# Kernel optimization log

Measured on AMD Instinct MI355X. Metric: run time of the kernel, lower is better.

## Reference

```python
import jax, jax.numpy as jnp
import numpy as np

B, S, D, H = 4, 2048, 1024, 16
NEG = -1e10  # matches the module's -10000000000.0 additive mask


def setup_inputs() -> dict:
    key = jax.random.key(0)
    k1, k2, k3, k4, k5 = jax.random.split(key, 5)
    scale = 0.02
    return {
        "x": jax.random.normal(k1, (B, S, D), dtype=jnp.float32),
        "w_qkv": jax.random.normal(k2, (D, 3 * D), dtype=jnp.float32) * scale,
        "b_qkv": jax.random.normal(k3, (3 * D,), dtype=jnp.float32) * scale,
        "w_out": jax.random.normal(k4, (D, D), dtype=jnp.float32) * scale,
        "b_out": jax.random.normal(k5, (D,), dtype=jnp.float32) * scale,
    }


def reference(x, w_qkv, b_qkv, w_out, b_out):
    b, s, d = x.shape
    hd = d // H  # per-head dim
    qkv = x @ w_qkv + b_qkv  # [b,s,3d]
    qq, kk, vv = jnp.split(qkv, 3, axis=-1)
    # [b,h,s,hd]
    qq = qq.reshape(b, s, H, hd).transpose(0, 2, 1, 3)
    kk = kk.reshape(b, s, H, hd).transpose(0, 2, 1, 3)
    vv = vv.reshape(b, s, H, hd).transpose(0, 2, 1, 3)
    scale = 1.0 / float(hd) ** 0.5
    # additive causal mask: NEG above diagonal, 0 on/below (as in module)
    mask = (1.0 - jnp.tri(s, dtype=jnp.float32)) * NEG
    attn = jnp.einsum("bhqd,bhkd->bhqk", qq, kk) * scale + mask
    attn = jax.nn.softmax(attn, axis=-1)
    out = jnp.einsum("bhqk,bhkd->bhqd", attn, vv)  # [b,h,s,hd]
    out = out.transpose(0, 2, 1, 3).reshape(b, s, d)
    return out @ w_out + b_out
```

## Files before the change

### kernel.cpp

```cpp
#include <hip/hip_runtime.h>
#include <hip/hip_bf16.h>
#include <stdint.h>


#define B_   4
#define S_   2048
#define D_   1024
#define H_   16
#define HD_  64
#define MTOK (B_ * S_)
#define BK   32
#define QSCALE 0.18033688011112042f

typedef __attribute__((ext_vector_type(8))) short bfx8;
typedef __attribute__((ext_vector_type(4))) float fx4;
typedef __attribute__((ext_vector_type(16))) float fx16;

static __device__ __forceinline__ unsigned short f2bf(float f) {
    union { float f; uint32_t u; } v{f};
    uint32_t u = v.u;
    u += 0x7fffu + ((u >> 16) & 1u);
    return (unsigned short)(u >> 16);
}

static __device__ __forceinline__ uint32_t cvtpk(float lo, float hi) {
    uint32_t r;
    asm volatile("v_cvt_pk_bf16_f32 %0, %1, %2" : "=v"(r) : "v"(lo), "v"(hi));
    return r;
}

static __device__ __forceinline__ void pswap(uint32_t& a, uint32_t& b) {
    asm volatile("v_permlane32_swap_b32 %0, %1" : "+v"(a), "+v"(b));
}

static __device__ __forceinline__ void gll16(const unsigned short* g, const unsigned short* l) {
    typedef const __attribute__((address_space(1))) void* gp_t;
    typedef __attribute__((address_space(3))) void* lp_t;
    __builtin_amdgcn_global_load_lds((gp_t)(uintptr_t)g, (lp_t)(uint32_t)(uintptr_t)l, 16, 0, 0);
}

__global__ void k_conv_x(const float* __restrict__ x, unsigned short* __restrict__ xb, int n8) {
    int i = blockIdx.x * blockDim.x + threadIdx.x;
    int stride = gridDim.x * blockDim.x;
    for (; i < n8; i += stride) {
        const float4* p = (const float4*)(x + (size_t)i * 8);
        float4 a = p[0], b = p[1];
        bfx8 o;
        o[0]=f2bf(a.x); o[1]=f2bf(a.y); o[2]=f2bf(a.z); o[3]=f2bf(a.w);
        o[4]=f2bf(b.x); o[5]=f2bf(b.y); o[6]=f2bf(b.z); o[7]=f2bf(b.w);
        *(bfx8*)(xb + (size_t)i * 8) = o;
    }
}

__global__ void k_transpose_bf(const float* __restrict__ w, unsigned short* __restrict__ wt,
                               int K, int N) {
    int idx = blockIdx.x * blockDim.x + threadIdx.x;
    int total = N * (K / 8);
    if (idx >= total) return;
    int n  = idx % N;
    int k0 = (idx / N) * 8;
    bfx8 o;
#pragma unroll
    for (int j = 0; j < 8; ++j) o[j] = f2bf(w[(size_t)(k0 + j) * N + n]);
    *(bfx8*)(wt + (size_t)n * K + k0) = o;
}

__global__ void k_transpose_v(const unsigned short* __restrict__ Vw,
                              unsigned short* __restrict__ Vt) {
    __shared__ unsigned short lds[64][72];
    const int bg = blockIdx.x;
    const int bh = bg >> 5;
    const int st = (bg & 31) * 64;
    const int t = threadIdx.x;
#pragma unroll
    for (int j = 0; j < 2; ++j) {
        int c = t + 256 * j;
        int row = c >> 3, q = c & 7;
        *(bfx8*)&lds[row][q * 8] = *(const bfx8*)&Vw[((size_t)bh * S_ + st + row) * HD_ + q * 8];
    }
    __syncthreads();
#pragma unroll
    for (int j = 0; j < 2; ++j) {
        int c = t + 256 * j;
        int d = c >> 3, q = c & 7;
        bfx8 o;
#pragma unroll
        for (int e = 0; e < 8; ++e) o[e] = lds[q * 8 + e][d];
        *(bfx8*)&Vt[((size_t)bh * HD_ + d) * S_ + st + q * 8] = o;
    }
}

__launch_bounds__(256)
__global__ void k_gemm_qkv(const unsigned short* __restrict__ A,
                           const unsigned short* __restrict__ Bt,
                           const float* __restrict__ bias,
                           unsigned short* __restrict__ Qw,
                           unsigned short* __restrict__ Kw,
                           unsigned short* __restrict__ Vw) {
    __shared__ unsigned short Al[128 * BK];
    __shared__ unsigned short Bl[128 * BK];
    const int wg = blockIdx.x;
    const int lin = (wg & 7) * 192 + (wg >> 3);
    const int ny = lin / 24, nx = lin - ny * 24;
    const int m0 = ny * 128;
    const int n0 = nx * 128;
    const int t = threadIdx.x;
    const int w = t >> 6, l = t & 63;
    const int wr = w >> 1, wc = w & 1;
    const int lr = l & 15, lg = l >> 4;
    const int srow = l >> 2;
    const int scol = (l & 3) * 8;
    fx4 acc[4][4] = {};

    for (int k0 = 0; k0 < D_; k0 += BK) {
        __syncthreads();
#pragma unroll
        for (int j = 0; j < 2; ++j) {
            int rb = j * 64 + w * 16;
            gll16(&A [(size_t)(m0 + rb + srow) * D_ + k0 + scol], &Al[rb * BK]);
            gll16(&Bt[(size_t)(n0 + rb + srow) * D_ + k0 + scol], &Bl[rb * BK]);
        }
        __syncthreads();
        bfx8 af[4], bf[4];
#pragma unroll
        for (int i = 0; i < 4; ++i) af[i] = *(const bfx8*)&Al[(wr * 64 + i * 16 + lr) * BK + lg * 8];
#pragma unroll
        for (int i = 0; i < 4; ++i) bf[i] = *(const bfx8*)&Bl[(wc * 64 + i * 16 + lr) * BK + lg * 8];
#pragma unroll
        for (int mi = 0; mi < 4; ++mi)
#pragma unroll
            for (int ni = 0; ni < 4; ++ni)
                acc[mi][ni] = __builtin_amdgcn_mfma_f32_16x16x32_bf16(bf[ni], af[mi], acc[mi][ni], 0, 0, 0);
    }

#pragma unroll
    for (int ni = 0; ni < 4; ++ni) {
        const int nn = n0 + wc * 64 + ni * 16 + lg * 4;
        const int mat = nn >> 10;
        const int h = (nn & 1023) >> 6, dd = nn & 63;
        const float4 bv = *(const float4*)&bias[nn];
        unsigned short* dst = (mat == 0) ? Qw : (mat == 1) ? Kw : Vw;
        const float sc = (mat == 0) ? QSCALE : 1.0f;
#pragma unroll
        for (int mi = 0; mi < 4; ++mi) {
            const int m = m0 + wr * 64 + mi * 16 + lr;
            const int b = m >> 11, s = m & 2047;
            const int bh = b * H_ + h;
            fx4 v = acc[mi][ni];
            float o0 = (v[0] + bv.x) * sc, o1 = (v[1] + bv.y) * sc;
            float o2 = (v[2] + bv.z) * sc, o3 = (v[3] + bv.w) * sc;
            uint2 u; u.x = cvtpk(o0, o1); u.y = cvtpk(o2, o3);
            *(uint2*)&dst[((size_t)bh * S_ + s) * HD_ + dd] = u;
        }
    }
}

__launch_bounds__(512, 4)
__global__ void k_attn(const unsigned short* __restrict__ Qw,
                       const unsigned short* __restrict__ Kw,
                       const unsigned short* __restrict__ Vt,
                       unsigned short* __restrict__ Ob) {
    __shared__ unsigned short Kl[2][64 * 64];
    __shared__ unsigned short Vl[2][64 * 64];
    const int wg = blockIdx.x;
    const int xcd = wg & 7, ix = wg >> 3;
    const int bh = xcd * 8 + (ix >> 3);
    const int pi = ix & 7;
    const int t = threadIdx.x;
    const int w = t >> 6, l = t & 63;
    const int lq = l & 31, hi = l >> 5;
    const int tile = (w < 4) ? (15 - pi) : pi;
    const int qr = tile * 128 + (w & 3) * 32;
    const int NT = 32 - 2 * pi;

    const unsigned short* Qp = Qw + (size_t)bh * S_ * HD_;
    const unsigned short* Kp = Kw + (size_t)bh * S_ * HD_;
    const unsigned short* Vp = Vt + (size_t)bh * HD_ * S_;

    bfx8 qf[4];
#pragma unroll
    for (int kb = 0; kb < 4; ++kb)
        qf[kb] = *(const bfx8*)&Qp[(size_t)(qr + lq) * HD_ + kb * 16 + hi * 8];

    fx16 oacc[2] = {};
    float mrow = -1e30f, lsum = 0.f;

    auto pvstep = [&](const uint32_t* pk, int s, int cb, int buf) {
        uint32_t w0 = pk[4 * s], w1 = pk[4 * s + 1], w2 = pk[4 * s + 2], w3 = pk[4 * s + 3];
        pswap(w0, w2);
        pswap(w1, w3);
        union { uint32_t u[4]; bfx8 v; } pf;
        pf.u[0] = w0; pf.u[1] = w1; pf.u[2] = w2; pf.u[3] = w3;
        bfx8 v0 = *(const bfx8*)((const char*)&Vl[buf][0] + lq * 128 + (cb ^ ((lq & 7) << 4)));
        bfx8 v1 = *(const bfx8*)((const char*)&Vl[buf][0] + (32 + lq) * 128 + (cb ^ ((lq & 7) << 4)));
        oacc[0] = __builtin_amdgcn_mfma_f32_32x32x16_bf16(v0, pf.v, oacc[0], 0, 0, 0);
        oacc[1] = __builtin_amdgcn_mfma_f32_32x32x16_bf16(v1, pf.v, oacc[1], 0, 0, 0);
    };

    {
        bfx8 sreg[2];
#pragma unroll
        for (int it = 0; it < 2; ++it) {
            int id = t + 512 * it;
            int c = id & 511;
            int row = c >> 3, q = c & 7;
            if (id < 512) sreg[it] = *(const bfx8*)&Kp[(size_t)row * HD_ + q * 8];
            else          sreg[it] = *(const bfx8*)&Vp[(size_t)row * S_ + q * 8];
        }
#pragma unroll
        for (int it = 0; it < 2; ++it) {
            int id = t + 512 * it;
            int c = id & 511;
            int row = c >> 3, q = c & 7;
            int off = row * 128 + ((q * 16) ^ ((row & 7) << 4));
            char* base = (id < 512) ? (char*)&Kl[0][0] : (char*)&Vl[0][0];
            *(bfx8*)(base + off) = sreg[it];
        }
    }
    __syncthreads();

    int buf = 0;
    for (int tkv = 0; tkv < NT; ++tkv) {
        const int kv0 = tkv * 64;
        const bool pre = (tkv + 1 < NT);
        bfx8 sreg[2];
        if (pre) {
            const int kn = kv0 + 64;
#pragma unroll
            for (int it = 0; it < 2; ++it) {
                int id = t + 512 * it;
                int c = id & 511;
                int row = c >> 3, q = c & 7;
                if (id < 512) sreg[it] = *(const bfx8*)&Kp[(size_t)(kn + row) * HD_ + q * 8];
                else          sreg[it] = *(const bfx8*)&Vp[(size_t)row * S_ + kn + q * 8];
            }
        }
        if (kv0 <= qr + 31) {
            fx16 s0 = {}, s1 = {};
            __builtin_amdgcn_s_setprio(1);
#pragma unroll
            for (int kb = 0; kb < 4; ++kb) {
                const int cb = kb * 32 + hi * 16;
                bfx8 k0 = *(const bfx8*)((const char*)&Kl[buf][0] + lq * 128 + (cb ^ ((lq & 7) << 4)));
                bfx8 k1 = *(const bfx8*)((const char*)&Kl[buf][0] + (32 + lq) * 128 + (cb ^ ((lq & 7) << 4)));
                s0 = __builtin_amdgcn_mfma_f32_32x32x16_bf16(k0, qf[kb], s0, 0, 0, 0);
                s1 = __builtin_amdgcn_mfma_f32_32x32x16_bf16(k1, qf[kb], s1, 0, 0, 0);
            }
            __builtin_amdgcn_s_setprio(0);
            if (kv0 + 63 > qr) {
                const int qrel = qr + lq - kv0;
#pragma unroll
                for (int r = 0; r < 16; ++r) {
                    const int kvo = (r & 3) + 8 * (r >> 2) + 4 * hi;
                    if (kvo > qrel)      s0[r] = -1e30f;
                    if (kvo + 32 > qrel) s1[r] = -1e30f;
                }
            }
            float mx = fmaxf(s0[0], s1[0]);
#pragma unroll
            for (int r = 1; r < 16; ++r) mx = fmaxf(mx, fmaxf(s0[r], s1[r]));
            mx = fmaxf(mx, __shfl_xor(mx, 32));
            if (!__all(mx <= mrow + 8.f)) {
                const float mnew = fmaxf(mrow, mx);
                const float al = exp2f(mrow - mnew);
                mrow = mnew;
#pragma unroll
                for (int r = 0; r < 16; ++r) { oacc[0][r] *= al; oacc[1][r] *= al; }
                lsum *= al;
            }
            uint32_t pk0[8], pk1[8];
            float ps = 0.f;
#pragma unroll
            for (int j = 0; j < 8; ++j) {
                float a0 = exp2f(s0[2 * j] - mrow), b0 = exp2f(s0[2 * j + 1] - mrow);
                float a1 = exp2f(s1[2 * j] - mrow), b1 = exp2f(s1[2 * j + 1] - mrow);
                ps += (a0 + b0) + (a1 + b1);
                pk0[j] = cvtpk(a0, b0);
                pk1[j] = cvtpk(a1, b1);
            }
            lsum += ps + __shfl_xor(ps, 32);
            __builtin_amdgcn_s_setprio(1);
            pvstep(pk0, 0, 0 * 32 + hi * 16, buf);
            pvstep(pk0, 1, 1 * 32 + hi * 16, buf);
            pvstep(pk1, 0, 2 * 32 + hi * 16, buf);
            pvstep(pk1, 1, 3 * 32 + hi * 16, buf);
            __builtin_amdgcn_s_setprio(0);
        }
        if (pre) {
#pragma unroll
            for (int it = 0; it < 2; ++it) {
                int id = t + 512 * it;
                int c = id & 511;
                int row = c >> 3, q = c & 7;
                int off = row * 128 + ((q * 16) ^ ((row & 7) << 4));
                char* base = (id < 512) ? (char*)&Kl[buf ^ 1][0] : (char*)&Vl[buf ^ 1][0];
                *(bfx8*)(base + off) = sreg[it];
            }
        }
        __syncthreads();
        buf ^= 1;
    }

    const int b = bh >> 4, h = bh & 15;
    const float iv = __builtin_amdgcn_rcpf(lsum);
    unsigned short* orow = Ob + ((size_t)b * S_ + qr + lq) * D_ + h * 64;
#pragma unroll
    for (int db = 0; db < 2; ++db)
#pragma unroll
        for (int rq = 0; rq < 4; ++rq) {
            uint2 u;
            u.x = cvtpk(oacc[db][rq * 4 + 0] * iv, oacc[db][rq * 4 + 1] * iv);
            u.y = cvtpk(oacc[db][rq * 4 + 2] * iv, oacc[db][rq * 4 + 3] * iv);
            *(uint2*)&orow[db * 32 + rq * 8 + hi * 4] = u;
        }
}

__launch_bounds__(256)
__global__ void k_gemm_proj(const unsigned short* __restrict__ A,
                            const unsigned short* __restrict__ Bt,
                            const float* __restrict__ bias,
                            float* __restrict__ out) {
    __shared__ unsigned short Al[128 * BK];
    __shared__ unsigned short Bl[128 * BK];
    const int wg = blockIdx.x;
    const int lin = (wg & 7) * 64 + (wg >> 3);
    const int ny = lin >> 3, nx = lin & 7;
    const int m0 = ny * 128;
    const int n0 = nx * 128;
    const int t = threadIdx.x;
    const int w = t >> 6, l = t & 63;
    const int wr = w >> 1, wc = w & 1;
    const int lr = l & 15, lg = l >> 4;
    const int srow = l >> 2;
    const int scol = (l & 3) * 8;
    fx4 acc[4][4] = {};

    for (int k0 = 0; k0 < D_; k0 += BK) {
        __syncthreads();
#pragma unroll
        for (int j = 0; j < 2; ++j) {
            int rb = j * 64 + w * 16;
            gll16(&A [(size_t)(m0 + rb + srow) * D_ + k0 + scol], &Al[rb * BK]);
            gll16(&Bt[(size_t)(n0 + rb + srow) * D_ + k0 + scol], &Bl[rb * BK]);
        }
        __syncthreads();
        bfx8 af[4], bf[4];
#pragma unroll
        for (int i = 0; i < 4; ++i) af[i] = *(const bfx8*)&Al[(wr * 64 + i * 16 + lr) * BK + lg * 8];
#pragma unroll
        for (int i = 0; i < 4; ++i) bf[i] = *(const bfx8*)&Bl[(wc * 64 + i * 16 + lr) * BK + lg * 8];
#pragma unroll
        for (int mi = 0; mi < 4; ++mi)
#pragma unroll
            for (int ni = 0; ni < 4; ++ni)
                acc[mi][ni] = __builtin_amdgcn_mfma_f32_16x16x32_bf16(bf[ni], af[mi], acc[mi][ni], 0, 0, 0);
    }
#pragma unroll
    for (int ni = 0; ni < 4; ++ni) {
        const int nn = n0 + wc * 64 + ni * 16 + lg * 4;
        const float4 bv = *(const float4*)&bias[nn];
#pragma unroll
        for (int mi = 0; mi < 4; ++mi) {
            const int m = m0 + wr * 64 + mi * 16 + lr;
            fx4 v = acc[mi][ni];
            float4 o; o.x = v[0] + bv.x; o.y = v[1] + bv.y; o.z = v[2] + bv.z; o.w = v[3] + bv.w;
            *(float4*)&out[(size_t)m * D_ + nn] = o;
        }
    }
}

extern "C" void kernel_launch(void* const* d_in, const int* in_sizes, int n_in,
                              void* d_out, int out_size, void* d_ws, size_t ws_size,
                              hipStream_t stream) {
    const float* x     = (const float*)d_in[0];
    const float* w_qkv = (const float*)d_in[1];
    const float* b_qkv = (const float*)d_in[2];
    const float* w_out = (const float*)d_in[3];
    const float* b_out = (const float*)d_in[4];
    float* out = (float*)d_out;

    unsigned short* xb    = (unsigned short*)d_ws;
    unsigned short* wqkvT = xb    + (size_t)MTOK * D_;
    unsigned short* woutT = wqkvT + (size_t)3 * D_ * D_;
    unsigned short* Qw    = woutT + (size_t)D_ * D_;
    unsigned short* Kw    = Qw    + (size_t)MTOK * D_;
    unsigned short* Vw    = Kw    + (size_t)MTOK * D_;
    unsigned short* attnb = Vw    + (size_t)MTOK * D_;
    unsigned short* Vt    = xb;

    k_conv_x<<<2048, 256, 0, stream>>>(x, xb, MTOK * D_ / 8);
    k_transpose_bf<<<(3 * D_ * (D_ / 8)) / 256, 256, 0, stream>>>(w_qkv, wqkvT, D_, 3 * D_);
    k_transpose_bf<<<(D_ * (D_ / 8)) / 256, 256, 0, stream>>>(w_out, woutT, D_, D_);
    k_gemm_qkv<<<1536, 256, 0, stream>>>(xb, wqkvT, b_qkv, Qw, Kw, Vw);
    k_transpose_v<<<2048, 256, 0, stream>>>(Vw, Vt);
    k_attn<<<512, 512, 0, stream>>>(Qw, Kw, Vt, attnb);
    k_gemm_proj<<<512, 256, 0, stream>>>(attnb, woutT, b_out, out);
}
```

Before: 204.3 us.

## Compute softmax row sums on MFMA and unroll attention loop with static buffers

The per-row softmax denominator is no longer accumulated with VALU adds and a cross-lane shuffle. It is now computed by an extra MFMA that multiplies the bf16 probability fragment by a ones vector, which moves that work onto the matrix cores. The KV loop is unrolled by two so the LDS double-buffer index is a compile-time constant, and the row max uses a 3-input max tree. The trade-off is one third more MFMA issue per tile in exchange for fewer VALU ops, which only pays off if softmax VALU work, not MFMA, is the bottleneck.

```diff
diff --git a/kernel.cpp b/kernel.cpp
--- a/kernel.cpp
+++ b/kernel.cpp
@@ -1,6 +1,7 @@
 #include <hip/hip_runtime.h>
 #include <hip/hip_bf16.h>
 #include <stdint.h>
+#include <type_traits>
 
 
 #define B_   4
@@ -15,6 +16,8 @@
 typedef __attribute__((ext_vector_type(8))) short bfx8;
 typedef __attribute__((ext_vector_type(4))) float fx4;
 typedef __attribute__((ext_vector_type(16))) float fx16;
+
+#define MAX3(a,b,c) fmaxf(fmaxf(a,b),c)
 
 static __device__ __forceinline__ unsigned short f2bf(float f) {
     union { float f; uint32_t u; } v{f};
@@ -160,8 +163,7 @@
                        const unsigned short* __restrict__ Kw,
                        const unsigned short* __restrict__ Vt,
                        unsigned short* __restrict__ Ob) {
-    __shared__ unsigned short Kl[2][64 * 64];
-    __shared__ unsigned short Vl[2][64 * 64];
+    __shared__ unsigned short Sh[4][64 * 64];
     const int wg = blockIdx.x;
     const int xcd = wg & 7, ix = wg >> 3;
     const int bh = xcd * 8 + (ix >> 3);
@@ -182,67 +184,41 @@
     for (int kb = 0; kb < 4; ++kb)
         qf[kb] = *(const bfx8*)&Qp[(size_t)(qr + lq) * HD_ + kb * 16 + hi * 8];
 
+    bfx8 ones;
+#pragma unroll
+    for (int j = 0; j < 8; ++j) ones[j] = (short)0x3F80;
+
     fx16 oacc[2] = {};
-    float mrow = -1e30f, lsum = 0.f;
-
-    auto pvstep = [&](const uint32_t* pk, int s, int cb, int buf) {
-        uint32_t w0 = pk[4 * s], w1 = pk[4 * s + 1], w2 = pk[4 * s + 2], w3 = pk[4 * s + 3];
-        pswap(w0, w2);
-        pswap(w1, w3);
-        union { uint32_t u[4]; bfx8 v; } pf;
-        pf.u[0] = w0; pf.u[1] = w1; pf.u[2] = w2; pf.u[3] = w3;
-        bfx8 v0 = *(const bfx8*)((const char*)&Vl[buf][0] + lq * 128 + (cb ^ ((lq & 7) << 4)));
-        bfx8 v1 = *(const bfx8*)((const char*)&Vl[buf][0] + (32 + lq) * 128 + (cb ^ ((lq & 7) << 4)));
-        oacc[0] = __builtin_amdgcn_mfma_f32_32x32x16_bf16(v0, pf.v, oacc[0], 0, 0, 0);
-        oacc[1] = __builtin_amdgcn_mfma_f32_32x32x16_bf16(v1, pf.v, oacc[1], 0, 0, 0);
-    };
-
-    {
-        bfx8 sreg[2];
-#pragma unroll
-        for (int it = 0; it < 2; ++it) {
-            int id = t + 512 * it;
-            int c = id & 511;
-            int row = c >> 3, q = c & 7;
-            if (id < 512) sreg[it] = *(const bfx8*)&Kp[(size_t)row * HD_ + q * 8];
-            else          sreg[it] = *(const bfx8*)&Vp[(size_t)row * S_ + q * 8];
-        }
-#pragma unroll
-        for (int it = 0; it < 2; ++it) {
-            int id = t + 512 * it;
-            int c = id & 511;
-            int row = c >> 3, q = c & 7;
-            int off = row * 128 + ((q * 16) ^ ((row & 7) << 4));
-            char* base = (id < 512) ? (char*)&Kl[0][0] : (char*)&Vl[0][0];
-            *(bfx8*)(base + off) = sreg[it];
-        }
-    }
-    __syncthreads();
-
-    int buf = 0;
-    for (int tkv = 0; tkv < NT; ++tkv) {
+    fx16 osum = {};
+    float mrow = -1e30f;
+
+    const int sid0 = t, sid1 = t + 512;
+    const int srow0 = (sid0 & 511) >> 3, sq0 = sid0 & 7;
+    const int srow1 = (sid1 & 511) >> 3, sq1 = sid1 & 7;
+    const int soff0 = srow0 * 128 + ((sq0 * 16) ^ ((srow0 & 7) << 4));
+    const int soff1 = srow1 * 128 + ((sq1 * 16) ^ ((srow1 & 7) << 4));
+
+    auto step = [&](auto bufc, int tkv) {
+        constexpr int BUF = decltype(bufc)::value;
         const int kv0 = tkv * 64;
         const bool pre = (tkv + 1 < NT);
-        bfx8 sreg[2];
+        bfx8 sreg0, sreg1;
         if (pre) {
             const int kn = kv0 + 64;
-#pragma unroll
-            for (int it = 0; it < 2; ++it) {
-                int id = t + 512 * it;
-                int c = id & 511;
-                int row = c >> 3, q = c & 7;
-                if (id < 512) sreg[it] = *(const bfx8*)&Kp[(size_t)(kn + row) * HD_ + q * 8];
-                else          sreg[it] = *(const bfx8*)&Vp[(size_t)row * S_ + kn + q * 8];
-            }
+            sreg0 = *(const bfx8*)&Kp[(size_t)(kn + srow0) * HD_ + sq0 * 8];
+            sreg1 = *(const bfx8*)&Vp[(size_t)srow1 * S_ + kn + sq1 * 8];
         }
         if (kv0 <= qr + 31) {
+            const char* Kb = (const char*)&Sh[BUF][0];
+            const char* Vb = (const char*)&Sh[2 + BUF][0];
+            const int sw = (lq & 7) << 4;
             fx16 s0 = {}, s1 = {};
             __builtin_amdgcn_s_setprio(1);
 #pragma unroll
             for (int kb = 0; kb < 4; ++kb) {
                 const int cb = kb * 32 + hi * 16;
-                bfx8 k0 = *(const bfx8*)((const char*)&Kl[buf][0] + lq * 128 + (cb ^ ((lq & 7) << 4)));
-                bfx8 k1 = *(const bfx8*)((const char*)&Kl[buf][0] + (32 + lq) * 128 + (cb ^ ((lq & 7) << 4)));
+                bfx8 k0 = *(const bfx8*)(Kb + lq * 128 + (cb ^ sw));
+                bfx8 k1 = *(const bfx8*)(Kb + (32 + lq) * 128 + (cb ^ sw));
                 s0 = __builtin_amdgcn_mfma_f32_32x32x16_bf16(k0, qf[kb], s0, 0, 0, 0);
                 s1 = __builtin_amdgcn_mfma_f32_32x32x16_bf16(k1, qf[kb], s1, 0, 0, 0);
             }
@@ -256,9 +232,22 @@
                     if (kvo + 32 > qrel) s1[r] = -1e30f;
                 }
             }
-            float mx = fmaxf(s0[0], s1[0]);
-#pragma unroll
-            for (int r = 1; r < 16; ++r) mx = fmaxf(mx, fmaxf(s0[r], s1[r]));
+            float a0 = MAX3(s0[0], s0[1], s0[2]);
+            float a1 = MAX3(s0[3], s0[4], s0[5]);
+            float a2 = MAX3(s0[6], s0[7], s0[8]);
+            float a3 = MAX3(s0[9], s0[10], s0[11]);
+            float a4 = MAX3(s0[12], s0[13], s0[14]);
+            float a5 = MAX3(s0[15], s1[0], s1[1]);
+            float a6 = MAX3(s1[2], s1[3], s1[4]);
+            float a7 = MAX3(s1[5], s1[6], s1[7]);
+            float a8 = MAX3(s1[8], s1[9], s1[10]);
+            float a9 = MAX3(s1[11], s1[12], s1[13]);
+            float aA = fmaxf(s1[14], s1[15]);
+            float b0 = MAX3(a0, a1, a2);
+            float b1 = MAX3(a3, a4, a5);
+            float b2 = MAX3(a6, a7, a8);
+            float b3 = fmaxf(a9, aA);
+            float mx = MAX3(fmaxf(b0, b1), b2, b3);
             mx = fmaxf(mx, __shfl_xor(mx, 32));
             if (!__all(mx <= mrow + 8.f)) {
                 const float mnew = fmaxf(mrow, mx);
@@ -266,43 +255,56 @@
                 mrow = mnew;
 #pragma unroll
                 for (int r = 0; r < 16; ++r) { oacc[0][r] *= al; oacc[1][r] *= al; }
-                lsum *= al;
+                osum[0] *= al;
             }
             uint32_t pk0[8], pk1[8];
-            float ps = 0.f;
 #pragma unroll
             for (int j = 0; j < 8; ++j) {
-                float a0 = exp2f(s0[2 * j] - mrow), b0 = exp2f(s0[2 * j + 1] - mrow);
-                float a1 = exp2f(s1[2 * j] - mrow), b1 = exp2f(s1[2 * j + 1] - mrow);
-                ps += (a0 + b0) + (a1 + b1);
-                pk0[j] = cvtpk(a0, b0);
-                pk1[j] = cvtpk(a1, b1);
+                pk0[j] = cvtpk(exp2f(s0[2 * j] - mrow), exp2f(s0[2 * j + 1] - mrow));
+                pk1[j] = cvtpk(exp2f(s1[2 * j] - mrow), exp2f(s1[2 * j + 1] - mrow));
             }
-            lsum += ps + __shfl_xor(ps, 32);
             __builtin_amdgcn_s_setprio(1);
-            pvstep(pk0, 0, 0 * 32 + hi * 16, buf);
-            pvstep(pk0, 1, 1 * 32 + hi * 16, buf);
-            pvstep(pk1, 0, 2 * 32 + hi * 16, buf);
-            pvstep(pk1, 1, 3 * 32 + hi * 16, buf);
+#pragma unroll
+            for (int sl = 0; sl < 4; ++sl) {
+                const uint32_t* pk = (sl < 2) ? pk0 : pk1;
+                const int s = sl & 1;
+                uint32_t w0 = pk[4 * s], w1 = pk[4 * s + 1], w2 = pk[4 * s + 2], w3 = pk[4 * s + 3];
+                pswap(w0, w2);
+                pswap(w1, w3);
+                union { uint32_t u[4]; bfx8 v; } pf;
+                pf.u[0] = w0; pf.u[1] = w1; pf.u[2] = w2; pf.u[3] = w3;
+                const int cb = sl * 32 + hi * 16;
+                bfx8 v0 = *(const bfx8*)(Vb + lq * 128 + (cb ^ sw));
+                bfx8 v1 = *(const bfx8*)(Vb + (32 + lq) * 128 + (cb ^ sw));
+                oacc[0] = __builtin_amdgcn_mfma_f32_32x32x16_bf16(v0, pf.v, oacc[0], 0, 0, 0);
+                oacc[1] = __builtin_amdgcn_mfma_f32_32x32x16_bf16(v1, pf.v, oacc[1], 0, 0, 0);
+                osum    = __builtin_amdgcn_mfma_f32_32x32x16_bf16(ones, pf.v, osum, 0, 0, 0);
+            }
             __builtin_amdgcn_s_setprio(0);
         }
         if (pre) {
-#pragma unroll
-            for (int it = 0; it < 2; ++it) {
-                int id = t + 512 * it;
-                int c = id & 511;
-                int row = c >> 3, q = c & 7;
-                int off = row * 128 + ((q * 16) ^ ((row & 7) << 4));
-                char* base = (id < 512) ? (char*)&Kl[buf ^ 1][0] : (char*)&Vl[buf ^ 1][0];
-                *(bfx8*)(base + off) = sreg[it];
-            }
-        }
-        __syncthreads();
-        buf ^= 1;
+            *(bfx8*)((char*)&Sh[BUF ^ 1][0] + soff0) = sreg0;
+            *(bfx8*)((char*)&Sh[2 + (BUF ^ 1)][0] + soff1) = sreg1;
+        }
+    };
+
+    {
+        bfx8 s0 = *(const bfx8*)&Kp[(size_t)srow0 * HD_ + sq0 * 8];
+        bfx8 s1 = *(const bfx8*)&Vp[(size_t)srow1 * S_ + sq1 * 8];
+        *(bfx8*)((char*)&Sh[0][0] + soff0) = s0;
+        *(bfx8*)((char*)&Sh[2][0] + soff1) = s1;
+    }
+    __syncthreads();
+
+    for (int tkv = 0; tkv < NT; tkv += 2) {
+        step(std::integral_constant<int, 0>{}, tkv);
+        __syncthreads();
+        step(std::integral_constant<int, 1>{}, tkv + 1);
+        __syncthreads();
     }
 
     const int b = bh >> 4, h = bh & 15;
-    const float iv = __builtin_amdgcn_rcpf(lsum);
+    const float iv = __builtin_amdgcn_rcpf(osum[0]);
     unsigned short* orow = Ob + ((size_t)b * S_ + qr + lq) * D_ + h * 64;
 #pragma unroll
     for (int db = 0; db < 2; ++db)
```

Result: slower. 223.2 us (+9.2%).
